# Kernel tuning notes

Hardware: AMD Instinct MI355X
Metric: run time of the kernel (lower is better)

## Reference

```python
import jax, jax.numpy as jnp
import numpy as np

D_MODEL, DFF, OUT, SEQ = 256, 1024, 32, 512
SIGMA = 0.1          # sigma for q/k/v/z SMC noise
SIGMA_OBS = 0.5      # observation noise


def _layernorm(x, g, b, eps=1e-6):
    mu = jnp.mean(x, axis=-1, keepdims=True)
    var = jnp.mean(jnp.square(x - mu), axis=-1, keepdims=True)
    return (x - mu) * jax.lax.rsqrt(var + eps) * g + b


def _resample(params, i_t, t):
    # params: (B,P,S,D); i_t: (B,P) ancestor indices; resample only the past [:t+1]
    past = jnp.take_along_axis(params[:, :, :t + 1, :], i_t[:, :, None, None], axis=1)
    return jnp.concatenate([past, params[:, :, t + 1:, :]], axis=2)


def setup_inputs() -> dict:
    key = jax.random.key(0)
    ks = jax.random.split(key, 24)
    B, P = 32, 10
    d = {
        'x': jax.random.normal(ks[0], (B, P, D_MODEL), jnp.float32),
        'y': jax.random.normal(ks[1], (B, P, OUT), jnp.float32),
        'K': jax.random.normal(ks[2], (B, P, SEQ, D_MODEL), jnp.float32),
        'V': jax.random.normal(ks[3], (B, P, SEQ, D_MODEL), jnp.float32),
        'R': jax.random.normal(ks[4], (B, P, SEQ, D_MODEL), jnp.float32),
        'noise_q': jax.random.normal(ks[5], (B, P, 1, D_MODEL), jnp.float32),
        'noise_k': jax.random.normal(ks[6], (B, P, 1, D_MODEL), jnp.float32),
        'noise_v': jax.random.normal(ks[7], (B, P, 1, D_MODEL), jnp.float32),
        'noise_z': jax.random.normal(ks[8], (B, P, 1, D_MODEL), jnp.float32),
        'dec_timestep': 256,
    }
    s = 0.02
    d['wq_w'] = jax.random.normal(ks[9], (D_MODEL, D_MODEL), jnp.float32) * s
    d['wq_b'] = jnp.zeros((D_MODEL,), jnp.float32)
    d['wk_w'] = jax.random.normal(ks[10], (D_MODEL, D_MODEL), jnp.float32) * s
    d['wk_b'] = jnp.zeros((D_MODEL,), jnp.float32)
    d['wv_w'] = jax.random.normal(ks[11], (D_MODEL, D_MODEL), jnp.float32) * s
    d['wv_b'] = jnp.zeros((D_MODEL,), jnp.float32)
    d['wz_w'] = jax.random.normal(ks[12], (D_MODEL, D_MODEL), jnp.float32) * s
    d['wz_b'] = jnp.zeros((D_MODEL,), jnp.float32)
    d['ln1_g'] = jnp.ones((D_MODEL,), jnp.float32)
    d['ln1_b'] = jnp.zeros((D_MODEL,), jnp.float32)
    d['ffn_w1'] = jax.random.normal(ks[13], (D_MODEL, DFF), jnp.float32) * s
    d['ffn_b1'] = jnp.zeros((DFF,), jnp.float32)
    d['ffn_w2'] = jax.random.normal(ks[14], (DFF, D_MODEL), jnp.float32) * s
    d['ffn_b2'] = jnp.zeros((D_MODEL,), jnp.float32)
    d['ln2_g'] = jnp.ones((D_MODEL,), jnp.float32)
    d['ln2_b'] = jnp.zeros((D_MODEL,), jnp.float32)
    d['out_w'] = jax.random.normal(ks[15], (D_MODEL, OUT), jnp.float32) * s
    d['out_b'] = jnp.zeros((OUT,), jnp.float32)
    return d


def reference(x, y, K, V, R, noise_q, noise_k, noise_v, noise_z,
              wq_w, wq_b, wk_w, wk_b, wv_w, wv_b, wz_w, wz_b,
              ln1_g, ln1_b, ffn_w1, ffn_b1, ffn_w2, ffn_b2,
              ln2_g, ln2_b, out_w, out_b, dec_timestep):
    t = dec_timestep
    B, P, D = x.shape
    sq = jnp.sqrt(jnp.float32(SIGMA))
    xq = x[:, :, None, :]           # (B,P,1,D)
    yq = y[:, :, None, :]           # (B,P,1,F_y)
    # --- Self_Attention_SMC: project current token, add SMC gaussian noise ---
    q = xq @ wq_w + wq_b + sq * noise_q
    k = xq @ wk_w + wk_b + sq * noise_k
    v = xq @ wv_w + wv_b + sq * noise_v
    # in-place style KV cache update at timestep t (concat past/new/future)
    K = jnp.concatenate([K[:, :, :t, :], k, K[:, :, t + 1:, :]], axis=2)
    V = jnp.concatenate([V[:, :, :t, :], v, V[:, :, t + 1:, :]], axis=2)
    logits = jnp.einsum('bpod,bpsd->bpos', q, K) / jnp.sqrt(jnp.float32(D))
    attn_weights = jax.nn.softmax(logits, axis=-1)          # (B,P,1,S)
    z = jnp.einsum('bpos,bpsd->bpod', attn_weights, V)
    z = z @ wz_w + wz_b + sq * noise_z
    # --- full_model: layernorm + FFN + layernorm ---
    out = _layernorm(z + xq, ln1_g, ln1_b)
    r = jax.nn.relu(out @ ffn_w1 + ffn_b1) @ ffn_w2 + ffn_b2
    r = _layernorm(r + out, ln2_g, ln2_b)                   # (B,P,1,D)
    predictions = r @ out_w + out_b                          # (B,P,1,F_y)
    R = jnp.concatenate([R[:, :, :t, :], r, R[:, :, t + 1:, :]], axis=2)
    mu = jnp.squeeze(yq - predictions, axis=-2)              # (B,P,F_y)
    log_w = -jnp.sum(mu * mu, axis=-1) / (2.0 * SIGMA_OBS)   # (B,P)
    w = jax.nn.softmax(jnp.exp(log_w), axis=-1)              # faithful to original (softmax of exp)
    w = jax.lax.stop_gradient(w)
    # categorical resampling of ancestors (tf.random.categorical uses w as logits)
    i_t = jax.random.categorical(jax.random.key(42), w[:, None, :], shape=(B, P))
    i_t = jax.lax.stop_gradient(i_t)
    K = _resample(K, i_t, t)
    V = _resample(V, i_t, t)
    R = _resample(R, i_t, t)
    return r, attn_weights, K, V, R, w
```

## Files before the change

### kernel.cpp

```cpp
#include <hip/hip_runtime.h>
#include <hip/hip_bf16.h>
#include <stdint.h>

#define BATCH 32
#define NPART 10
#define BP_TOT 320
#define DM 256
#define FF 1024
#define OD 32
#define SL 512
#define NCHUNK 8
#define CROWS 64

#define SQRT_SIGMA 0.31622776601683794f

__device__ __forceinline__ uint32_t rotl32(uint32_t x, uint32_t r) {
    return (x << r) | (x >> (32u - r));
}

__device__ __forceinline__ void threefry2x32(uint32_t k0, uint32_t k1,
                                             uint32_t x0, uint32_t x1,
                                             uint32_t& o0, uint32_t& o1) {
    uint32_t k2 = k0 ^ k1 ^ 0x1BD11BDAu;
    uint32_t x = x0 + k0, y = x1 + k1;
#define TFR(r) { x += y; y = rotl32(y, r); y ^= x; }
    TFR(13u) TFR(15u) TFR(26u) TFR(6u)
    x += k1; y += k2 + 1u;
    TFR(17u) TFR(29u) TFR(16u) TFR(24u)
    x += k2; y += k0 + 2u;
    TFR(13u) TFR(15u) TFR(26u) TFR(6u)
    x += k0; y += k1 + 3u;
    TFR(17u) TFR(29u) TFR(16u) TFR(24u)
    x += k1; y += k2 + 4u;
    TFR(13u) TFR(15u) TFR(26u) TFR(6u)
    x += k2; y += k0 + 5u;
#undef TFR
    o0 = x; o1 = y;
}

__device__ __forceinline__ float jax_gumbel_part(uint32_t m) {
    const float TINY = 1.17549435e-38f;
    uint32_t o0, o1;
    threefry2x32(0u, 42u, 0u, m, o0, o1);
    uint32_t bits = o0 ^ o1;
    uint32_t fb = (bits >> 9) | 0x3f800000u;
    float f = __uint_as_float(fb) - 1.0f;
    float u = fmaxf(TINY, f + TINY);
    return -logf(-logf(u));
}

__global__ __launch_bounds__(256) void qkv_kernel(
    const float* __restrict__ x,
    const float* __restrict__ nq, const float* __restrict__ nk,
    const float* __restrict__ nv,
    const float* __restrict__ wq_w, const float* __restrict__ wq_b,
    const float* __restrict__ wk_w, const float* __restrict__ wk_b,
    const float* __restrict__ wv_w, const float* __restrict__ wv_b,
    float* __restrict__ qtmp, float* __restrict__ knew, float* __restrict__ vnew)
{
    const int bb = blockIdx.x;
    const int m  = blockIdx.y;
    const int d  = threadIdx.x;

    __shared__ float xs[4][DM];
    #pragma unroll
    for (int g = 0; g < 4; ++g) xs[g][d] = x[(bb * 4 + g) * DM + d];
    __syncthreads();

    const float* W; const float* bias; const float* noise;
    if (m == 0)      { W = wq_w; bias = wq_b; noise = nq; }
    else if (m == 1) { W = wk_w; bias = wk_b; noise = nk; }
    else             { W = wv_w; bias = wv_b; noise = nv; }

    float a0 = 0.f, a1 = 0.f, a2 = 0.f, a3 = 0.f;
    #pragma unroll 4
    for (int i = 0; i < DM; ++i) {
        float wv = W[i * DM + d];
        a0 = fmaf(xs[0][i], wv, a0);
        a1 = fmaf(xs[1][i], wv, a1);
        a2 = fmaf(xs[2][i], wv, a2);
        a3 = fmaf(xs[3][i], wv, a3);
    }
    float r[4] = {a0, a1, a2, a3};
    #pragma unroll
    for (int g = 0; g < 4; ++g) {
        int bp = bb * 4 + g;
        float v = r[g] + bias[d] + SQRT_SIGMA * noise[bp * DM + d];
        if (m == 0)      qtmp[(size_t)bp * SL + d] = v;
        else if (m == 1) knew[(size_t)bp * DM + d] = v;
        else             vnew[(size_t)bp * DM + d] = v;
    }
}

__global__ __launch_bounds__(256) void attn_chunk_kernel(
    const float* __restrict__ Kin, const float* __restrict__ Vin,
    const float* __restrict__ knew, const float* __restrict__ vnew,
    const float* __restrict__ qtmp, const int* __restrict__ t_ptr,
    float* __restrict__ Kout, float* __restrict__ Vout,
    float* __restrict__ logits, float* __restrict__ zpart,
    float* __restrict__ mstat)
{
    const int bp   = blockIdx.x;
    const int sc   = blockIdx.y;
    const int tid  = threadIdx.x;
    const int lane = tid & 63;
    const int wave = tid >> 6;
    const int t    = *t_ptr;

    __shared__ float qs[DM], ks[DM], vs[DM];
    __shared__ float att_loc[CROWS];
    __shared__ float scratch[4 * 256];
    __shared__ float redm[1], rede[1];

    qs[tid] = qtmp[(size_t)bp * SL + tid];
    ks[tid] = knew[(size_t)bp * DM + tid];
    vs[tid] = vnew[(size_t)bp * DM + tid];
    __syncthreads();

    const float* Kbp = Kin + (size_t)bp * SL * DM;
    const float* Vbp = Vin + (size_t)bp * SL * DM;
    float4 q4 = *(const float4*)&qs[lane * 4];
    const int s0 = sc * CROWS + wave * 16;

    for (int j0 = 0; j0 < 16; j0 += 8) {
        float4 k4[8];
        #pragma unroll
        for (int u = 0; u < 8; ++u) {
            int s = s0 + j0 + u;
            k4[u] = (s == t) ? *(const float4*)&ks[lane * 4]
                             : *(const float4*)&Kbp[(size_t)s * DM + lane * 4];
        }
        #pragma unroll
        for (int u = 0; u < 8; ++u) {
            int s = s0 + j0 + u;
            if (s > t) *(float4*)(Kout + ((size_t)bp * SL + s) * DM + lane * 4) = k4[u];
            float acc = q4.x * k4[u].x + q4.y * k4[u].y + q4.z * k4[u].z + q4.w * k4[u].w;
            #pragma unroll
            for (int off = 32; off; off >>= 1) acc += __shfl_down(acc, off);
            if (lane == 0) {
                float l = acc * 0.0625f;
                att_loc[wave * 16 + j0 + u] = l;
                logits[(size_t)bp * SL + s] = l;
            }
        }
    }
    __syncthreads();

    if (wave == 0) {
        float l = att_loc[lane];
        float mm = l;
        #pragma unroll
        for (int off = 32; off; off >>= 1) mm = fmaxf(mm, __shfl_down(mm, off));
        if (lane == 0) redm[0] = mm;
    }
    __syncthreads();
    const float m_loc = redm[0];
    if (wave == 0) {
        float p = expf(att_loc[lane] - m_loc);
        att_loc[lane] = p;
        float e = p;
        #pragma unroll
        for (int off = 32; off; off >>= 1) e += __shfl_down(e, off);
        if (lane == 0) rede[0] = e;
    }
    __syncthreads();
    const float e_loc = rede[0];

    float4 z4 = make_float4(0.f, 0.f, 0.f, 0.f);
    for (int j0 = 0; j0 < 16; j0 += 8) {
        float4 v4[8];
        #pragma unroll
        for (int u = 0; u < 8; ++u) {
            int s = s0 + j0 + u;
            v4[u] = (s == t) ? *(const float4*)&vs[lane * 4]
                             : *(const float4*)&Vbp[(size_t)s * DM + lane * 4];
        }
        #pragma unroll
        for (int u = 0; u < 8; ++u) {
            int s = s0 + j0 + u;
            if (s > t) *(float4*)(Vout + ((size_t)bp * SL + s) * DM + lane * 4) = v4[u];
            float a = att_loc[wave * 16 + j0 + u];
            z4.x = fmaf(a, v4[u].x, z4.x);
            z4.y = fmaf(a, v4[u].y, z4.y);
            z4.z = fmaf(a, v4[u].z, z4.z);
            z4.w = fmaf(a, v4[u].w, z4.w);
        }
    }
    *(float4*)&scratch[wave * 256 + lane * 4] = z4;
    __syncthreads();
    if (tid < DM) {
        float zp = (scratch[tid] + scratch[256 + tid]) + (scratch[512 + tid] + scratch[768 + tid]);
        zpart[((size_t)bp * NCHUNK + sc) * DM + tid] = zp;
    }
    if (tid == 0) {
        mstat[((size_t)bp * NCHUNK + sc) * 2 + 0] = m_loc;
        mstat[((size_t)bp * NCHUNK + sc) * 2 + 1] = e_loc;
    }
}

__global__ __launch_bounds__(1024) void post_kernel(
    const float* __restrict__ x, const float* __restrict__ nz,
    const float* __restrict__ logits, const float* __restrict__ zpart,
    const float* __restrict__ mstat,
    const float* __restrict__ wz_w, const float* __restrict__ wz_b,
    const float* __restrict__ ln1_g, const float* __restrict__ ln1_b,
    const float* __restrict__ w1, const float* __restrict__ b1,
    const float* __restrict__ w2, const float* __restrict__ b2,
    const float* __restrict__ ln2_g, const float* __restrict__ ln2_b,
    float* __restrict__ attn_out, float* __restrict__ r_out)
{
    const int bp   = blockIdx.x;
    const int tid  = threadIdx.x;
    const int lane = tid & 63;
    const int wave = tid >> 6;
    const int grp  = tid >> 8;
    const int qtid = tid & 255;

    __shared__ float buf[DM];
    __shared__ float xs[DM];
    __shared__ float hid[FF];
    __shared__ float scratch[1024];
    __shared__ float red[32];

    const float* ms = mstat + (size_t)bp * (2 * NCHUNK);
    float mc[NCHUNK], ec[NCHUNK];
    float gm = -3.402823466e+38f;
    #pragma unroll
    for (int c = 0; c < NCHUNK; ++c) {
        mc[c] = ms[2 * c]; ec[c] = ms[2 * c + 1];
        gm = fmaxf(gm, mc[c]);
    }
    float fc[NCHUNK], denom = 0.f;
    #pragma unroll
    for (int c = 0; c < NCHUNK; ++c) {
        fc[c] = expf(mc[c] - gm);
        denom = fmaf(ec[c], fc[c], denom);
    }
    const float inv = 1.0f / denom;

    if (tid < 512) {
        float l = logits[(size_t)bp * SL + tid];
        attn_out[(size_t)bp * SL + tid] = expf(l - gm) * inv;
    } else if (tid < 768) {
        int d = tid - 512;
        const float* zp = zpart + (size_t)bp * NCHUNK * DM;
        float z = 0.f;
        #pragma unroll
        for (int c = 0; c < NCHUNK; ++c) z = fmaf(zp[c * DM + d], fc[c], z);
        buf[d] = z * inv;
    } else {
        int d = tid - 768;
        xs[d] = x[bp * DM + d];
    }
    __syncthreads();

    {
        const int i0 = grp * 64;
        float a0 = 0.f, a1 = 0.f;
        #pragma unroll 4
        for (int ii = 0; ii < 32; ++ii) {
            a0 = fmaf(buf[i0 + ii],      wz_w[(i0 + ii)      * DM + qtid], a0);
            a1 = fmaf(buf[i0 + ii + 32], wz_w[(i0 + ii + 32) * DM + qtid], a1);
        }
        scratch[grp * 256 + qtid] = a0 + a1;
    }
    __syncthreads();
    float h = 0.f;
    if (tid < DM) {
        float az = (scratch[tid] + scratch[256 + tid]) + (scratch[512 + tid] + scratch[768 + tid]);
        h = az + wz_b[tid] + SQRT_SIGMA * nz[bp * DM + tid] + xs[tid];
    }

    float s1 = h;
    #pragma unroll
    for (int off = 32; off; off >>= 1) s1 += __shfl_down(s1, off);
    if (lane == 0) red[wave] = s1;
    __syncthreads();
    float mu = (red[0] + red[1] + red[2] + red[3]) * (1.0f / DM);
    float dv = (tid < DM) ? (h - mu) : 0.f;
    float s2 = dv * dv;
    #pragma unroll
    for (int off = 32; off; off >>= 1) s2 += __shfl_down(s2, off);
    if (lane == 0) red[16 + wave] = s2;
    __syncthreads();
    float var = (red[16] + red[17] + red[18] + red[19]) * (1.0f / DM);
    float o = 0.f;
    __syncthreads();
    if (tid < DM) {
        o = dv * rsqrtf(var + 1e-6f) * ln1_g[tid] + ln1_b[tid];
        buf[tid] = o;
    }
    __syncthreads();

    {
        float h0 = 0.f, h1 = 0.f, h2 = 0.f, h3 = 0.f;
        #pragma unroll 4
        for (int i = 0; i < 64; ++i) {
            h0 = fmaf(buf[i],       w1[(i      ) * FF + tid], h0);
            h1 = fmaf(buf[i +  64], w1[(i +  64) * FF + tid], h1);
            h2 = fmaf(buf[i + 128], w1[(i + 128) * FF + tid], h2);
            h3 = fmaf(buf[i + 192], w1[(i + 192) * FF + tid], h3);
        }
        hid[tid] = fmaxf((h0 + h1) + (h2 + h3) + b1[tid], 0.f);
    }
    __syncthreads();

    {
        const int i0 = grp * 256;
        float a0 = 0.f, a1 = 0.f, a2 = 0.f, a3 = 0.f;
        #pragma unroll 4
        for (int ii = 0; ii < 64; ++ii) {
            a0 = fmaf(hid[i0 + ii],       w2[(i0 + ii      ) * DM + qtid], a0);
            a1 = fmaf(hid[i0 + ii +  64], w2[(i0 + ii +  64) * DM + qtid], a1);
            a2 = fmaf(hid[i0 + ii + 128], w2[(i0 + ii + 128) * DM + qtid], a2);
            a3 = fmaf(hid[i0 + ii + 192], w2[(i0 + ii + 192) * DM + qtid], a3);
        }
        scratch[grp * 256 + qtid] = (a0 + a1) + (a2 + a3);
    }
    __syncthreads();
    float rr = 0.f;
    if (tid < DM) {
        rr = (scratch[tid] + scratch[256 + tid]) + (scratch[512 + tid] + scratch[768 + tid])
           + b2[tid] + o;
    }

    float t1 = rr;
    #pragma unroll
    for (int off = 32; off; off >>= 1) t1 += __shfl_down(t1, off);
    if (lane == 0) red[wave] = t1;
    __syncthreads();
    float mu2 = (red[0] + red[1] + red[2] + red[3]) * (1.0f / DM);
    float dv2 = (tid < DM) ? (rr - mu2) : 0.f;
    float t2 = dv2 * dv2;
    #pragma unroll
    for (int off = 32; off; off >>= 1) t2 += __shfl_down(t2, off);
    if (lane == 0) red[16 + wave] = t2;
    __syncthreads();
    float var2 = (red[16] + red[17] + red[18] + red[19]) * (1.0f / DM);
    if (tid < DM) {
        float rf = dv2 * rsqrtf(var2 + 1e-6f) * ln2_g[tid] + ln2_b[tid];
        r_out[(size_t)bp * DM + tid] = rf;
    }
}

__global__ __launch_bounds__(320) void weights_kernel(
    const float* __restrict__ r, const float* __restrict__ y,
    const float* __restrict__ out_w, const float* __restrict__ out_b,
    float* __restrict__ w_out, int* __restrict__ i_t)
{
    const int b   = blockIdx.x;
    const int tid = threadIdx.x;
    const int p   = tid >> 5;
    const int j   = tid & 31;

    __shared__ float sred[NPART];
    __shared__ float es[NPART];
    __shared__ float pe[NPART];
    __shared__ float wsm[NPART];

    const float* rrow = r + (size_t)(b * NPART + p) * DM;
    float acc = 0.f;
    #pragma unroll 4
    for (int i = 0; i < DM; ++i) acc = fmaf(rrow[i], out_w[i * OD + j], acc);
    float pred = acc + out_b[j];
    float muv  = y[(size_t)(b * NPART + p) * OD + j] - pred;
    float s    = muv * muv;
    #pragma unroll
    for (int off = 16; off; off >>= 1) s += __shfl_down(s, off, 32);
    if (j == 0) sred[p] = s;
    __syncthreads();

    if (tid < NPART) es[tid] = expf(-sred[tid]);
    __syncthreads();
    if (tid < NPART) {
        float mx = es[0];
        #pragma unroll
        for (int i = 1; i < NPART; ++i) mx = fmaxf(mx, es[i]);
        pe[tid] = expf(es[tid] - mx);
    }
    __syncthreads();
    if (tid < NPART) {
        float sum = 0.f;
        #pragma unroll
        for (int i = 0; i < NPART; ++i) sum += pe[i];
        float wv = pe[tid] / sum;
        w_out[b * NPART + tid] = wv;
        wsm[tid] = wv;
    }
    __syncthreads();

    if (tid < NPART) {
        int pp = tid;
        int best = 0;
        float bests = -3.402823466e+38f;
        #pragma unroll
        for (int jj = 0; jj < NPART; ++jj) {
            uint32_t m = (uint32_t)(b * 100 + pp * 10 + jj);
            float score = jax_gumbel_part(m) + wsm[jj];
            if (score > bests) { bests = score; best = jj; }
        }
        i_t[b * NPART + pp] = best;
    }
}

__global__ __launch_bounds__(256) void resample_kernel(
    const float* __restrict__ Kin, const float* __restrict__ Vin,
    const float* __restrict__ Rin,
    const float* __restrict__ knew, const float* __restrict__ vnew,
    const float* __restrict__ rnew,
    const int* __restrict__ i_t, const int* __restrict__ t_ptr,
    float* __restrict__ Kout, float* __restrict__ Vout, float* __restrict__ Rout)
{
    const int t    = *t_ptr;
    const int ysel = blockIdx.y;
    const int tid  = threadIdx.x;
    size_t idx  = (size_t)blockIdx.x * 256 + tid;
    int lane4 = (int)(idx & 63);
    int row   = (int)(idx >> 6);
    int bpi   = row >> 9;
    int s     = row & 511;

    if (ysel != 2 && s > t) return;

    int b     = bpi / NPART;
    int p     = bpi - b * NPART;
    int srcp  = (s <= t) ? i_t[bpi] : p;
    int src_bpi = b * NPART + srcp;

    const float* src;
    if (s == t) {
        const float* nb = (ysel == 1) ? knew : (ysel == 0) ? vnew : rnew;
        src = nb + (size_t)src_bpi * DM;
    } else {
        const float* base = (ysel == 1) ? Kin : (ysel == 0) ? Vin : Rin;
        src = base + ((size_t)src_bpi * SL + s) * DM;
    }
    float* outb = (ysel == 1) ? Kout : (ysel == 0) ? Vout : Rout;
    float4 v4 = *(const float4*)(src + (size_t)lane4 * 4);
    *(float4*)(outb + (size_t)row * DM + (size_t)lane4 * 4) = v4;
}

extern "C" void kernel_launch(void* const* d_in, const int* in_sizes, int n_in,
                              void* d_out, int out_size, void* d_ws, size_t ws_size,
                              hipStream_t stream) {
    const float* x    = (const float*)d_in[0];
    const float* y    = (const float*)d_in[1];
    const float* Kin  = (const float*)d_in[2];
    const float* Vin  = (const float*)d_in[3];
    const float* Rin  = (const float*)d_in[4];
    const float* nq   = (const float*)d_in[5];
    const float* nk   = (const float*)d_in[6];
    const float* nv   = (const float*)d_in[7];
    const float* nz   = (const float*)d_in[8];
    const int*   tptr = (const int*)d_in[9];
    const float* wq_w = (const float*)d_in[10];
    const float* wq_b = (const float*)d_in[11];
    const float* wk_w = (const float*)d_in[12];
    const float* wk_b = (const float*)d_in[13];
    const float* wv_w = (const float*)d_in[14];
    const float* wv_b = (const float*)d_in[15];
    const float* wz_w = (const float*)d_in[16];
    const float* wz_b = (const float*)d_in[17];
    const float* ln1g = (const float*)d_in[18];
    const float* ln1b = (const float*)d_in[19];
    const float* w1   = (const float*)d_in[20];
    const float* b1   = (const float*)d_in[21];
    const float* w2   = (const float*)d_in[22];
    const float* b2   = (const float*)d_in[23];
    const float* ln2g = (const float*)d_in[24];
    const float* ln2b = (const float*)d_in[25];
    const float* outw = (const float*)d_in[26];
    const float* outb = (const float*)d_in[27];

    float* out = (float*)d_out;
    const size_t R_ELEMS    = (size_t)BP_TOT * DM;
    const size_t ATTN_ELEMS = (size_t)BP_TOT * SL;
    const size_t KVR_ELEMS  = (size_t)BP_TOT * SL * DM;
    float* r_out    = out;
    float* attn_out = out + R_ELEMS;
    float* K_out    = out + R_ELEMS + ATTN_ELEMS;
    float* V_out    = K_out + KVR_ELEMS;
    float* R_out    = V_out + KVR_ELEMS;
    float* w_out    = R_out + KVR_ELEMS;

    float* knew = (float*)d_ws;
    float* vnew = knew + R_ELEMS;
    int*   i_t  = (int*)(vnew + R_ELEMS);

    float* logits = R_out;
    float* zpart  = R_out + ATTN_ELEMS;
    float* mstat  = zpart + (size_t)BP_TOT * NCHUNK * DM;

    qkv_kernel<<<dim3(BP_TOT / 4, 3), 256, 0, stream>>>(
        x, nq, nk, nv, wq_w, wq_b, wk_w, wk_b, wv_w, wv_b,
        attn_out, knew, vnew);

    attn_chunk_kernel<<<dim3(BP_TOT, NCHUNK), 256, 0, stream>>>(
        Kin, Vin, knew, vnew, attn_out, tptr,
        K_out, V_out, logits, zpart, mstat);

    post_kernel<<<BP_TOT, 1024, 0, stream>>>(
        x, nz, logits, zpart, mstat,
        wz_w, wz_b, ln1g, ln1b, w1, b1, w2, b2, ln2g, ln2b,
        attn_out, r_out);

    weights_kernel<<<BATCH, 320, 0, stream>>>(
        r_out, y, outw, outb, w_out, i_t);

    resample_kernel<<<dim3(163840 / 4, 3), 256, 0, stream>>>(
        Kin, Vin, Rin, knew, vnew, r_out, i_t, tptr,
        K_out, V_out, R_out);
}
```

Before: 346.6 us.

## Use nontemporal stores, halve attention chunks, double work per resample thread

Output copies of K, V, R and the attention weights now use nontemporal stores, so streaming writes are meant to pollute the cache less. The attention kernel splits the sequence into 4 chunks of 128 rows instead of 8 of 64, and its max and sum reductions are rewritten as a two-wave reduction. The resample kernel handles two float4 per thread with half as many blocks. Fewer chunks mean fewer blocks and less partial-result traffic, at the cost of less parallelism per particle.

```diff
diff --git a/kernel.cpp b/kernel.cpp
--- a/kernel.cpp
+++ b/kernel.cpp
@@ -9,10 +9,18 @@
 #define FF 1024
 #define OD 32
 #define SL 512
-#define NCHUNK 8
-#define CROWS 64
+#define NCHUNK 4
+#define CROWS 128
 
 #define SQRT_SIGMA 0.31622776601683794f
+
+typedef float nfloat4 __attribute__((ext_vector_type(4)));
+
+__device__ __forceinline__ void nt_store4(const float4& v, float* p) {
+    nfloat4 nv;
+    nv.x = v.x; nv.y = v.y; nv.z = v.z; nv.w = v.w;
+    __builtin_nontemporal_store(nv, (nfloat4*)p);
+}
 
 __device__ __forceinline__ uint32_t rotl32(uint32_t x, uint32_t r) {
     return (x << r) | (x >> (32u - r));
@@ -110,19 +118,21 @@
     __shared__ float qs[DM], ks[DM], vs[DM];
     __shared__ float att_loc[CROWS];
     __shared__ float scratch[4 * 256];
-    __shared__ float redm[1], rede[1];
-
-    qs[tid] = qtmp[(size_t)bp * SL + tid];
-    ks[tid] = knew[(size_t)bp * DM + tid];
-    vs[tid] = vnew[(size_t)bp * DM + tid];
+    __shared__ float redm[2], rede[2];
+
+    if (tid < DM) {
+        qs[tid] = qtmp[(size_t)bp * SL + tid];
+        ks[tid] = knew[(size_t)bp * DM + tid];
+        vs[tid] = vnew[(size_t)bp * DM + tid];
+    }
     __syncthreads();
 
     const float* Kbp = Kin + (size_t)bp * SL * DM;
     const float* Vbp = Vin + (size_t)bp * SL * DM;
     float4 q4 = *(const float4*)&qs[lane * 4];
-    const int s0 = sc * CROWS + wave * 16;
-
-    for (int j0 = 0; j0 < 16; j0 += 8) {
+    const int s0 = sc * CROWS + wave * 32;
+
+    for (int j0 = 0; j0 < 32; j0 += 8) {
         float4 k4[8];
         #pragma unroll
         for (int u = 0; u < 8; ++u) {
@@ -133,41 +143,38 @@
         #pragma unroll
         for (int u = 0; u < 8; ++u) {
             int s = s0 + j0 + u;
-            if (s > t) *(float4*)(Kout + ((size_t)bp * SL + s) * DM + lane * 4) = k4[u];
+            if (s > t)
+                nt_store4(k4[u], Kout + ((size_t)bp * SL + s) * DM + lane * 4);
             float acc = q4.x * k4[u].x + q4.y * k4[u].y + q4.z * k4[u].z + q4.w * k4[u].w;
             #pragma unroll
             for (int off = 32; off; off >>= 1) acc += __shfl_down(acc, off);
             if (lane == 0) {
                 float l = acc * 0.0625f;
-                att_loc[wave * 16 + j0 + u] = l;
+                att_loc[wave * 32 + j0 + u] = l;
                 logits[(size_t)bp * SL + s] = l;
             }
         }
     }
     __syncthreads();
 
-    if (wave == 0) {
-        float l = att_loc[lane];
-        float mm = l;
-        #pragma unroll
-        for (int off = 32; off; off >>= 1) mm = fmaxf(mm, __shfl_down(mm, off));
-        if (lane == 0) redm[0] = mm;
-    }
-    __syncthreads();
-    const float m_loc = redm[0];
-    if (wave == 0) {
-        float p = expf(att_loc[lane] - m_loc);
-        att_loc[lane] = p;
-        float e = p;
-        #pragma unroll
-        for (int off = 32; off; off >>= 1) e += __shfl_down(e, off);
-        if (lane == 0) rede[0] = e;
-    }
-    __syncthreads();
-    const float e_loc = rede[0];
+    float l = (tid < CROWS) ? att_loc[tid] : -3.402823466e+38f;
+    float mm = l;
+    #pragma unroll
+    for (int off = 32; off; off >>= 1) mm = fmaxf(mm, __shfl_down(mm, off));
+    if (tid < CROWS && lane == 0) redm[wave] = mm;
+    __syncthreads();
+    const float m_loc = fmaxf(redm[0], redm[1]);
+    float p = (tid < CROWS) ? expf(l - m_loc) : 0.f;
+    if (tid < CROWS) att_loc[tid] = p;
+    float e = p;
+    #pragma unroll
+    for (int off = 32; off; off >>= 1) e += __shfl_down(e, off);
+    if (tid < CROWS && lane == 0) rede[wave] = e;
+    __syncthreads();
+    const float e_loc = rede[0] + rede[1];
 
     float4 z4 = make_float4(0.f, 0.f, 0.f, 0.f);
-    for (int j0 = 0; j0 < 16; j0 += 8) {
+    for (int j0 = 0; j0 < 32; j0 += 8) {
         float4 v4[8];
         #pragma unroll
         for (int u = 0; u < 8; ++u) {
@@ -178,8 +185,9 @@
         #pragma unroll
         for (int u = 0; u < 8; ++u) {
             int s = s0 + j0 + u;
-            if (s > t) *(float4*)(Vout + ((size_t)bp * SL + s) * DM + lane * 4) = v4[u];
-            float a = att_loc[wave * 16 + j0 + u];
+            if (s > t)
+                nt_store4(v4[u], Vout + ((size_t)bp * SL + s) * DM + lane * 4);
+            float a = att_loc[wave * 32 + j0 + u];
             z4.x = fmaf(a, v4[u].x, z4.x);
             z4.y = fmaf(a, v4[u].y, z4.y);
             z4.z = fmaf(a, v4[u].z, z4.z);
@@ -240,7 +248,8 @@
 
     if (tid < 512) {
         float l = logits[(size_t)bp * SL + tid];
-        attn_out[(size_t)bp * SL + tid] = expf(l - gm) * inv;
+        __builtin_nontemporal_store(expf(l - gm) * inv,
+                                    attn_out + (size_t)bp * SL + tid);
     } else if (tid < 768) {
         int d = tid - 512;
         const float* zp = zpart + (size_t)bp * NCHUNK * DM;
@@ -414,30 +423,31 @@
     const int t    = *t_ptr;
     const int ysel = blockIdx.y;
     const int tid  = threadIdx.x;
-    size_t idx  = (size_t)blockIdx.x * 256 + tid;
-    int lane4 = (int)(idx & 63);
-    int row   = (int)(idx >> 6);
-    int bpi   = row >> 9;
-    int s     = row & 511;
-
-    if (ysel != 2 && s > t) return;
-
-    int b     = bpi / NPART;
-    int p     = bpi - b * NPART;
-    int srcp  = (s <= t) ? i_t[bpi] : p;
-    int src_bpi = b * NPART + srcp;
-
-    const float* src;
-    if (s == t) {
-        const float* nb = (ysel == 1) ? knew : (ysel == 0) ? vnew : rnew;
-        src = nb + (size_t)src_bpi * DM;
-    } else {
-        const float* base = (ysel == 1) ? Kin : (ysel == 0) ? Vin : Rin;
-        src = base + ((size_t)src_bpi * SL + s) * DM;
-    }
-    float* outb = (ysel == 1) ? Kout : (ysel == 0) ? Vout : Rout;
-    float4 v4 = *(const float4*)(src + (size_t)lane4 * 4);
-    *(float4*)(outb + (size_t)row * DM + (size_t)lane4 * 4) = v4;
+
+    const float* gat = (ysel == 1) ? Kin : (ysel == 0) ? Vin : Rin;
+    const float* nb  = (ysel == 1) ? knew : (ysel == 0) ? vnew : rnew;
+    float* outb      = (ysel == 1) ? Kout : (ysel == 0) ? Vout : Rout;
+
+    #pragma unroll
+    for (int half = 0; half < 2; ++half) {
+        size_t f4i = (size_t)blockIdx.x * 512 + half * 256 + tid;
+        int lane4 = (int)(f4i & 63);
+        int row   = (int)(f4i >> 6);
+        int bpi   = row >> 9;
+        int s     = row & 511;
+
+        if (ysel != 2 && s > t) continue;
+
+        int b     = bpi / NPART;
+        int p     = bpi - b * NPART;
+        int srcp  = (s <= t) ? i_t[bpi] : p;
+        int src_bpi = b * NPART + srcp;
+
+        const float* src = (s == t) ? nb + (size_t)src_bpi * DM
+                                    : gat + ((size_t)src_bpi * SL + s) * DM;
+        float4 v4 = *(const float4*)(src + (size_t)lane4 * 4);
+        nt_store4(v4, outb + (size_t)row * DM + (size_t)lane4 * 4);
+    }
 }
 
 extern "C" void kernel_launch(void* const* d_in, const int* in_sizes, int n_in,
@@ -507,7 +517,7 @@
     weights_kernel<<<BATCH, 320, 0, stream>>>(
         r_out, y, outw, outb, w_out, i_t);
 
-    resample_kernel<<<dim3(163840 / 4, 3), 256, 0, stream>>>(
+    resample_kernel<<<dim3(163840 / 8, 3), 256, 0, stream>>>(
         Kin, Vin, Rin, knew, vnew, r_out, i_t, tptr,
         K_out, V_out, R_out);
 }
```

Result: faster. 329.5 us (-5.0%).
